# Kernel tuning notes

Hardware: AMD Instinct MI355X
Metric: run time of the kernel (lower is better)

The kernel has to match this reference:

```python
import jax, jax.numpy as jnp
import numpy as np

B, T, D, K = 64, 4096, 90, 32
LOG2PI = 1.8378770664093453


def setup_inputs() -> dict:
    key = jax.random.key(0)
    k1, k2, k3, k4, k5 = jax.random.split(key, 5)
    X = jax.random.normal(k1, (B, T, D), dtype=jnp.float32)
    state_priors = jax.random.uniform(k2, (K,), dtype=jnp.float32)
    transition_matrix = jax.random.uniform(k3, (K, K), dtype=jnp.float32)
    mu = jax.random.normal(k4, (K, D), dtype=jnp.float32) * 0.5
    log_var = jax.random.normal(k5, (K, D), dtype=jnp.float32) * 0.1
    return {"X": X, "state_priors": state_priors,
            "transition_matrix": transition_matrix, "mu": mu, "log_var": log_var}


def _emission_logprobs(X, mu, log_var):
    # Diagonal-Gaussian log density per state: (B,T,K)
    # expand (x-mu)^2*inv_var to avoid materializing a (B,T,K,D) tensor
    inv_var = jnp.exp(-log_var)                                   # (K,D)
    quad = (jnp.einsum('btd,kd->btk', X * X, inv_var)
            - 2.0 * jnp.einsum('btd,kd->btk', X, mu * inv_var)
            + jnp.sum(mu * mu * inv_var, axis=-1))                # (B,T,K)
    return -0.5 * (quad + jnp.sum(log_var, axis=-1) + D * LOG2PI)


def reference(X, state_priors, transition_matrix, mu, log_var):
    log_A = jax.nn.log_softmax(transition_matrix, axis=1)   # (K,K)
    log_pi = jax.nn.log_softmax(state_priors, axis=0)       # (K,)
    em = _emission_logprobs(X, mu, log_var)                 # (B,T,K)

    log_alpha0 = log_pi + em[:, 0, :]                       # (B,K)

    def step(log_alpha, e_t):
        # log_alpha: (B,K), e_t: (B,K)
        la = e_t + jax.nn.logsumexp(log_alpha[:, :, None] + log_A[None], axis=1)
        return la, None

    em_rest = jnp.swapaxes(em[:, 1:, :], 0, 1)              # (T-1,B,K)
    log_alpha_T, _ = jax.lax.scan(step, log_alpha0, em_rest)
    # sum over subjects of logsumexp over states at final timestep
    return jnp.sum(jax.nn.logsumexp(log_alpha_T, axis=-1))
```

## Files before the change

### kernel.cpp

```cpp
#include <hip/hip_runtime.h>
#include <stdint.h>

#define B_ 64
#define T_ 4096
#define D_ 90
#define K_ 32
#define CH_ 32
#define F_  128
#define NB_ 2048

typedef float f32x16 __attribute__((ext_vector_type(16)));
typedef __bf16 bf16x8 __attribute__((ext_vector_type(8)));

#define WS_A     0
#define WS_PI    1024
#define WS_C0    1056
#define WS_WF    1088
#define WS_EACC  4160
#define WS_MS    12352
#define WS_E0    20544
#define WS_Q2    22080

__device__ __forceinline__ int perm_r(int r) {
  int t2 = (r >> 2) & 3;
  return r + ((t2 == 1) ? 4 : (t2 == 2) ? -4 : 0);
}
__device__ __forceinline__ uint32_t pk2(float hi, float lo) {
  return __builtin_amdgcn_perm(__float_as_uint(hi), __float_as_uint(lo), 0x07060302u);
}
__device__ __forceinline__ uint32_t rnd_pk(float hi, float lo) {
  uint32_t uh = __float_as_uint(hi) + 0x8000u;
  uint32_t ul = __float_as_uint(lo) + 0x8000u;
  return __builtin_amdgcn_perm(uh, ul, 0x07060302u);
}
__device__ __forceinline__ float bf2f(ushort u) {
  return __uint_as_float(((uint32_t)u) << 16);
}
__device__ __forceinline__ bf16x8 mkbf(uint32_t a, uint32_t b, uint32_t c, uint32_t d) {
  union { uint32_t u[4]; bf16x8 v; } x;
  x.u[0] = a; x.u[1] = b; x.u[2] = c; x.u[3] = d;
  return x.v;
}

__global__ __launch_bounds__(1024) void prep_kernel(
    const float* __restrict__ priors, const float* __restrict__ trans,
    const float* __restrict__ mu, const float* __restrict__ lv,
    float* __restrict__ ws) {
  int tid = threadIdx.x;
  {
    float v = trans[tid];
    float m = v;
    #pragma unroll
    for (int mk = 16; mk; mk >>= 1) m = fmaxf(m, __shfl_xor(m, mk));
    float e = expf(v - m);
    float s = e;
    #pragma unroll
    for (int mk = 16; mk; mk >>= 1) s += __shfl_xor(s, mk);
    ws[WS_A + tid] = e / s;
  }
  if (tid < 32) {
    float v = priors[tid];
    float m = v;
    #pragma unroll
    for (int mk = 16; mk; mk >>= 1) m = fmaxf(m, __shfl_xor(m, mk));
    float e = expf(v - m);
    float s = e;
    #pragma unroll
    for (int mk = 16; mk; mk >>= 1) s += __shfl_xor(s, mk);
    ws[WS_PI + tid] = e / s;
  }
  for (int i = tid; i < 6144; i += 1024) {
    int j = i & 7, l = (i >> 3) & 63, cm = i >> 9;
    int c = cm >> 1, mat = cm & 1;
    int h = l >> 5, nn = l & 31;
    int d = 16 * c + 8 * h + j;
    float v = 0.0f;
    if (d < D_) {
      float ivd = expf(-lv[nn * D_ + d]);
      v = (mat == 0) ? -0.5f * ivd : mu[nn * D_ + d] * ivd;
    }
    ((ushort*)(ws + WS_WF))[i] = (ushort)((__float_as_uint(v) + 0x8000u) >> 16);
  }
  if (tid < 32) {
    float s = 0.0f;
    for (int d = 0; d < D_; ++d) {
      float l  = lv[tid * D_ + d];
      float iv = expf(-l);
      float m_ = mu[tid * D_ + d];
      s += m_ * m_ * iv + l;
    }
    ws[WS_C0 + tid] = -0.5f * (s + (float)D_ * 1.8378770664093453f);
  }
}

__global__ __launch_bounds__(256, 8) void fused_kernel(const float* __restrict__ X,
                                                       float* __restrict__ ws,
                                                       float* __restrict__ out) {
  __shared__ __align__(16) ushort sh[4][1280];
  __shared__ float msb[4];
  __shared__ int   peb[4];
  int tid = threadIdx.x;
  int l = tid & 63, w = tid >> 6;
  int n = l & 31, h = l >> 5;
  int tB = blockIdx.x << 7;
  int t0 = tB + (w << 5);
  int b  = t0 >> 12;
  if (blockIdx.x == 0 && tid == 0) *out = 0.0f;

  const float* xr = X + (size_t)(t0 + n) * D_;
  const uint4* wfp = (const uint4*)((const ushort*)(ws + WS_WF));
  float c0 = ws[WS_C0 + n];
  f32x16 acc1, acc2;
  #pragma unroll
  for (int r = 0; r < 16; ++r) { acc1[r] = 0.0f; acc2[r] = 0.0f; }
  #pragma unroll
  for (int c = 0; c < 6; ++c) {
    int s = 16 * c + 8 * h;
    union { uint32_t u[4]; bf16x8 v; } xb, x2b;
    #pragma unroll
    for (int p = 0; p < 4; ++p) {
      float2 v2;
      if (s + 2 * p < D_) v2 = *(const float2*)(xr + s + 2 * p);
      else { v2.x = 0.0f; v2.y = 0.0f; }
      xb.u[p]  = rnd_pk(v2.y, v2.x);
      x2b.u[p] = rnd_pk(v2.y * v2.y, v2.x * v2.x);
    }
    union { uint4 u; bf16x8 v; } w1, w2;
    w2.u = wfp[(2 * c) * 64 + l];
    w1.u = wfp[(2 * c + 1) * 64 + l];
    acc1 = __builtin_amdgcn_mfma_f32_32x32x16_bf16(xb.v,  w1.v, acc1, 0, 0, 0);
    acc2 = __builtin_amdgcn_mfma_f32_32x32x16_bf16(x2b.v, w2.v, acc2, 0, 0, 0);
  }
  float em[16], mrow[16];
  #pragma unroll
  for (int r = 0; r < 16; ++r) {
    float v = acc1[r] + acc2[r] + c0;
    em[r] = v;
    float m = v;
    #pragma unroll
    for (int mk = 1; mk <= 16; mk <<= 1) m = fmaxf(m, __shfl_xor(m, mk));
    mrow[r] = m;
  }
  ushort* Ew = sh[w];
  #pragma unroll
  for (int q = 0; q < 4; ++q) {
    float e0 = exp2f((em[4*q]   - mrow[4*q])   * 1.44269504088896f);
    float e1 = exp2f((em[4*q+1] - mrow[4*q+1]) * 1.44269504088896f);
    float e2 = exp2f((em[4*q+2] - mrow[4*q+2]) * 1.44269504088896f);
    float e3 = exp2f((em[4*q+3] - mrow[4*q+3]) * 1.44269504088896f);
    uint2 d;
    d.x = rnd_pk(e1, e0);
    d.y = rnd_pk(e3, e2);
    *(uint2*)(Ew + n * 40 + 8 * q + 4 * h) = d;
    if (q == 0 && h == 0 && (t0 & (T_ - 1)) == 0)
      ((ushort*)(ws + WS_E0))[b * K_ + n] = (ushort)(d.x & 0xFFFF);
  }
  float msum = 0.0f;
  #pragma unroll
  for (int r = 0; r < 16; ++r) msum += mrow[r];
  msum += __shfl_xor(msum, 32);
  if (l == 0) msb[w] = msum;

  int col = perm_r(n);
  const float* A = ws + WS_A;
  float astat[16];
  #pragma unroll
  for (int j = 0; j < 8; ++j) {
    astat[j]     = A[(8 * h + j) * K_ + col];
    astat[8 + j] = A[(16 + 8 * h + j) * K_ + col];
  }
  uint32_t q[8];
  #pragma unroll
  for (int r = 0; r < 4; ++r) {
    int s0 = 8 * h + 2 * r;
    uint32_t lo = (s0 == n)     ? 0x3F80u : 0u;
    uint32_t hi = (s0 + 1 == n) ? 0x3F80u : 0u;
    q[r] = lo | (hi << 16);
    int s2 = s0 + 16;
    lo = (s2 == n)     ? 0x3F80u : 0u;
    hi = (s2 + 1 == n) ? 0x3F80u : 0u;
    q[4 + r] = lo | (hi << 16);
  }
  int eacc = 0;
  const f32x16 z = {0.f,0.f,0.f,0.f,0.f,0.f,0.f,0.f,0.f,0.f,0.f,0.f,0.f,0.f,0.f,0.f};
  f32x16 acc;
  #pragma unroll
  for (int r = 0; r < 16; ++r) acc[r] = 0.0f;

  auto step = [&](float e0) {
    uint32_t au[8];
    #pragma unroll
    for (int r = 0; r < 4; ++r) {
      au[r]     = pk2(astat[2 * r + 1] * e0, astat[2 * r] * e0);
      au[4 + r] = pk2(astat[8 + 2 * r + 1] * e0, astat[8 + 2 * r] * e0);
    }
    bf16x8 alo = mkbf(au[0], au[1], au[2], au[3]);
    bf16x8 ahi = mkbf(au[4], au[5], au[6], au[7]);
    bf16x8 qlo = mkbf(q[0], q[1], q[2], q[3]);
    bf16x8 qhi = mkbf(q[4], q[5], q[6], q[7]);
    acc = __builtin_amdgcn_mfma_f32_32x32x16_bf16(alo, qlo, z, 0, 0, 0);
    acc = __builtin_amdgcn_mfma_f32_32x32x16_bf16(ahi, qhi, acc, 0, 0, 0);
    #pragma unroll
    for (int r = 0; r < 4; ++r) {
      q[r]     = pk2(acc[2 * r + 1], acc[2 * r]);
      q[4 + r] = pk2(acc[8 + 2 * r + 1], acc[8 + 2 * r]);
    }
  };
  auto lmul = [&](uint4 lo, uint4 hi) {
    bf16x8 alo = mkbf(lo.x, lo.y, lo.z, lo.w);
    bf16x8 ahi = mkbf(hi.x, hi.y, hi.z, hi.w);
    bf16x8 qlo = mkbf(q[0], q[1], q[2], q[3]);
    bf16x8 qhi = mkbf(q[4], q[5], q[6], q[7]);
    acc = __builtin_amdgcn_mfma_f32_32x32x16_bf16(alo, qlo, z, 0, 0, 0);
    acc = __builtin_amdgcn_mfma_f32_32x32x16_bf16(ahi, qhi, acc, 0, 0, 0);
    #pragma unroll
    for (int r = 0; r < 4; ++r) {
      q[r]     = pk2(acc[2 * r + 1], acc[2 * r]);
      q[4 + r] = pk2(acc[8 + 2 * r + 1], acc[8 + 2 * r]);
    }
  };
  auto renorm = [&]() {
    float m = acc[0];
    #pragma unroll
    for (int r = 1; r < 16; ++r) m = fmaxf(m, acc[r]);
    #pragma unroll
    for (int mk = 1; mk <= 32; mk <<= 1) m = fmaxf(m, __shfl_xor(m, mk));
    int ex;
    frexpf(m, &ex);
    float sc = ldexpf(1.0f, -ex);
    eacc += ex;
    #pragma unroll
    for (int r = 0; r < 16; ++r) acc[r] *= sc;
    #pragma unroll
    for (int r = 0; r < 4; ++r) {
      q[r]     = pk2(acc[2 * r + 1], acc[2 * r]);
      q[4 + r] = pk2(acc[8 + 2 * r + 1], acc[8 + 2 * r]);
    }
  };

  const ushort* Eb = sh[w] + col * 40;
  int g0 = 0;
  if ((t0 & (T_ - 1)) == 0) {
    uint4 ev = *(const uint4*)(Eb);
    #pragma unroll
    for (int j = 1; j < 8; ++j) {
      uint32_t u = ((const uint32_t*)&ev)[j >> 1];
      step(bf2f((j & 1) ? (ushort)(u >> 16) : (ushort)(u & 0xFFFF)));
    }
    renorm();
    g0 = 1;
  }
  for (int g = g0; g < CH_ / 8; ++g) {
    uint4 ev = *(const uint4*)(Eb + 8 * g);
    #pragma unroll
    for (int j = 0; j < 8; ++j) {
      uint32_t u = ((const uint32_t*)&ev)[j >> 1];
      step(bf2f((j & 1) ? (ushort)(u >> 16) : (ushort)(u & 0xFFFF)));
    }
    renorm();
  }
  ushort* Qw = sh[w];
  #pragma unroll
  for (int r = 0; r < 16; ++r) {
    int m_ = (r & 3) + 8 * (r >> 2) + 4 * h;
    Qw[perm_r(m_) * 40 + n] = (ushort)(__float_as_uint(acc[r]) >> 16);
  }
  if (l == 0) peb[w] = eacc;
  __syncthreads();
  if (w != 0) return;

  #pragma unroll
  for (int r = 0; r < 4; ++r) {
    int s0 = 8 * h + 2 * r;
    uint32_t lo = (s0 == n)     ? 0x3F80u : 0u;
    uint32_t hi = (s0 + 1 == n) ? 0x3F80u : 0u;
    q[r] = lo | (hi << 16);
    int s2 = s0 + 16;
    lo = (s2 == n)     ? 0x3F80u : 0u;
    hi = (s2 + 1 == n) ? 0x3F80u : 0u;
    q[4 + r] = lo | (hi << 16);
  }
  eacc = peb[0] + peb[1] + peb[2] + peb[3];
  float msm = msb[0] + msb[1] + msb[2] + msb[3];
  #pragma unroll
  for (int p = 0; p < 4; ++p) {
    const ushort* base = sh[p] + col * 40;
    uint4 lo = *(const uint4*)(base + 8 * h);
    uint4 hi = *(const uint4*)(base + 16 + 8 * h);
    lmul(lo, hi);
  }
  renorm();
  ushort* Qo = (ushort*)(ws + WS_Q2) + (size_t)blockIdx.x * (K_ * K_);
  #pragma unroll
  for (int r = 0; r < 16; ++r) {
    int m_ = (r & 3) + 8 * (r >> 2) + 4 * h;
    Qo[perm_r(m_) * K_ + n] = (ushort)(__float_as_uint(acc[r]) >> 16);
  }
  if (l == 0) {
    ((int*)ws)[WS_EACC + blockIdx.x] = eacc;
    ws[WS_MS + blockIdx.x] = msm;
  }
}

__global__ __launch_bounds__(256) void combine_kernel(float* __restrict__ ws,
                                                      float* __restrict__ out) {
  __shared__ __align__(16) ushort pm[4][1280];
  __shared__ int pe[4];
  int tid = threadIdx.x;
  int l = tid & 63, w = tid >> 6;
  int h = l >> 5, n = l & 31;
  int b = blockIdx.x;
  int row = perm_r(n);
  int eacc;
  {
    const int* ea = ((const int*)ws) + WS_EACC + b * 32 + w * 8;
    int v = (l < 8) ? ea[l] : 0;
    #pragma unroll
    for (int mk = 1; mk <= 4; mk <<= 1) v += __shfl_xor(v, mk);
    eacc = __shfl(v, 0);
  }
  uint32_t q[8];
  #pragma unroll
  for (int r = 0; r < 4; ++r) {
    int s0 = 8 * h + 2 * r;
    uint32_t lo = (s0 == n)     ? 0x3F80u : 0u;
    uint32_t hi = (s0 + 1 == n) ? 0x3F80u : 0u;
    q[r] = lo | (hi << 16);
    int s2 = s0 + 16;
    lo = (s2 == n)     ? 0x3F80u : 0u;
    hi = (s2 + 1 == n) ? 0x3F80u : 0u;
    q[4 + r] = lo | (hi << 16);
  }
  f32x16 acc;
  #pragma unroll
  for (int r = 0; r < 16; ++r) acc[r] = 0.0f;
  const f32x16 z = {0.f,0.f,0.f,0.f,0.f,0.f,0.f,0.f,0.f,0.f,0.f,0.f,0.f,0.f,0.f,0.f};

  auto lmul = [&](uint4 lo, uint4 hi) {
    bf16x8 alo = mkbf(lo.x, lo.y, lo.z, lo.w);
    bf16x8 ahi = mkbf(hi.x, hi.y, hi.z, hi.w);
    bf16x8 qlo = mkbf(q[0], q[1], q[2], q[3]);
    bf16x8 qhi = mkbf(q[4], q[5], q[6], q[7]);
    acc = __builtin_amdgcn_mfma_f32_32x32x16_bf16(alo, qlo, z, 0, 0, 0);
    acc = __builtin_amdgcn_mfma_f32_32x32x16_bf16(ahi, qhi, acc, 0, 0, 0);
    #pragma unroll
    for (int r = 0; r < 4; ++r) {
      q[r]     = pk2(acc[2 * r + 1], acc[2 * r]);
      q[4 + r] = pk2(acc[8 + 2 * r + 1], acc[8 + 2 * r]);
    }
  };
  auto renorm = [&]() {
    float m = acc[0];
    #pragma unroll
    for (int r = 1; r < 16; ++r) m = fmaxf(m, acc[r]);
    #pragma unroll
    for (int mk = 1; mk <= 32; mk <<= 1) m = fmaxf(m, __shfl_xor(m, mk));
    int ex;
    frexpf(m, &ex);
    float sc = ldexpf(1.0f, -ex);
    eacc += ex;
    #pragma unroll
    for (int r = 0; r < 16; ++r) acc[r] *= sc;
    #pragma unroll
    for (int r = 0; r < 4; ++r) {
      q[r]     = pk2(acc[2 * r + 1], acc[2 * r]);
      q[4 + r] = pk2(acc[8 + 2 * r + 1], acc[8 + 2 * r]);
    }
  };

  const ushort* Qb = (const ushort*)(ws + WS_Q2) + (size_t)(b * 32 + w * 8) * (K_ * K_);
  #pragma unroll
  for (int p = 0; p < 8; ++p) {
    const ushort* Mc = Qb + (size_t)p * (K_ * K_) + row * K_;
    uint4 lo = *(const uint4*)(Mc + 8 * h);
    uint4 hi = *(const uint4*)(Mc + 16 + 8 * h);
    lmul(lo, hi);
    if ((p & 3) == 3) renorm();
  }
  #pragma unroll
  for (int r = 0; r < 16; ++r) {
    int m_ = (r & 3) + 8 * (r >> 2) + 4 * h;
    pm[w][perm_r(m_) * 40 + n] = (ushort)(__float_as_uint(acc[r]) >> 16);
  }
  if (l == 0) pe[w] = eacc;
  __syncthreads();
  if (w != 0) return;

  float alpha0 = ws[WS_PI + n] * bf2f(((const ushort*)(ws + WS_E0))[b * K_ + n]);
  float msm;
  {
    float v = (l < 32) ? ws[WS_MS + b * 32 + l] : 0.0f;
    #pragma unroll
    for (int mk = 1; mk <= 32; mk <<= 1) v += __shfl_xor(v, mk);
    msm = v;
  }
  #pragma unroll
  for (int r = 0; r < 4; ++r) {
    int s0 = 8 * h + 2 * r;
    uint32_t lo = (s0 == n)     ? 0x3F80u : 0u;
    uint32_t hi = (s0 + 1 == n) ? 0x3F80u : 0u;
    q[r] = lo | (hi << 16);
    int s2 = s0 + 16;
    lo = (s2 == n)     ? 0x3F80u : 0u;
    hi = (s2 + 1 == n) ? 0x3F80u : 0u;
    q[4 + r] = lo | (hi << 16);
  }
  #pragma unroll
  for (int r = 0; r < 16; ++r) acc[r] = 0.0f;
  int et = pe[0] + pe[1] + pe[2] + pe[3];
  #pragma unroll
  for (int p = 0; p < 4; ++p) {
    const ushort* base = pm[p] + row * 40;
    uint4 lo = *(const uint4*)(base + 8 * h);
    uint4 hi = *(const uint4*)(base + 16 + 8 * h);
    lmul(lo, hi);
  }
  float part = 0.0f;
  #pragma unroll
  for (int r = 0; r < 16; ++r) part += acc[r];
  part *= alpha0;
  #pragma unroll
  for (int mk = 1; mk <= 32; mk <<= 1) part += __shfl_xor(part, mk);
  if (l == 0) {
    float res = logf(part) + (float)et * 0.69314718055994531f + msm;
    atomicAdd(out, res);
  }
}

extern "C" void kernel_launch(void* const* d_in, const int* in_sizes, int n_in,
                              void* d_out, int out_size, void* d_ws, size_t ws_size,
                              hipStream_t stream) {
  (void)in_sizes; (void)n_in; (void)out_size; (void)ws_size;
  const float* X      = (const float*)d_in[0];
  const float* priors = (const float*)d_in[1];
  const float* trans  = (const float*)d_in[2];
  const float* mu     = (const float*)d_in[3];
  const float* lv     = (const float*)d_in[4];
  float* ws  = (float*)d_ws;
  float* out = (float*)d_out;
  prep_kernel<<<1, 1024, 0, stream>>>(priors, trans, mu, lv, ws);
  fused_kernel<<<NB_, 256, 0, stream>>>(X, ws, out);
  combine_kernel<<<B_, 256, 0, stream>>>(ws, out);
}
```

Measured before the change: 192.6 us.

## Stage X and emission weights through LDS with coalesced loads, shuffle emissions

The emission GEMM now copies the bf16 weight fragments into LDS once per block and stages X through a per-wave LDS buffer using coalesced row-pair loads, double-buffered against the MFMAs. X squared is recomputed from the bf16 values, and the two accumulators are merged into one. The per-step emission values are delivered by cross-lane shuffles from registers instead of an LDS round trip. This aims to fix strided, uncoalesced global reads of X and the repeated weight fetches. In exchange it adds block-wide barriers, more LDS use, and slightly different rounding of x^2, which is now computed from the bf16-rounded x.

```diff
diff --git a/kernel.cpp b/kernel.cpp
--- a/kernel.cpp
+++ b/kernel.cpp
@@ -20,6 +20,10 @@
 #define WS_MS    12352
 #define WS_E0    20544
 #define WS_Q2    22080
+
+#define LDS_XOFF(w) ((w) * 768)
+#define LDS_WF      3072
+#define LDS_TOT     9216
 
 __device__ __forceinline__ int perm_r(int r) {
   int t2 = (r >> 2) & 3;
@@ -96,7 +100,7 @@
 __global__ __launch_bounds__(256, 8) void fused_kernel(const float* __restrict__ X,
                                                        float* __restrict__ ws,
                                                        float* __restrict__ out) {
-  __shared__ __align__(16) ushort sh[4][1280];
+  __shared__ __align__(16) ushort sh[LDS_TOT];
   __shared__ float msb[4];
   __shared__ int   peb[4];
   int tid = threadIdx.x;
@@ -107,59 +111,96 @@
   int b  = t0 >> 12;
   if (blockIdx.x == 0 && tid == 0) *out = 0.0f;
 
-  const float* xr = X + (size_t)(t0 + n) * D_;
-  const uint4* wfp = (const uint4*)((const ushort*)(ws + WS_WF));
+  {
+    const uint4* wfp = (const uint4*)((const ushort*)(ws + WS_WF));
+    uint4* wfl = (uint4*)(sh + LDS_WF);
+    #pragma unroll
+    for (int k = 0; k < 3; ++k) wfl[tid + (k << 8)] = wfp[tid + (k << 8)];
+  }
   float c0 = ws[WS_C0 + n];
-  f32x16 acc1, acc2;
-  #pragma unroll
-  for (int r = 0; r < 16; ++r) { acc1[r] = 0.0f; acc2[r] = 0.0f; }
+
+  int srow = l >> 1, sp = l & 1;
+  const float* xg = X + (size_t)(t0 + srow) * D_ + 8 * sp;
+  ushort* xbuf = sh + LDS_XOFF(w);
+  float2 va[4];
+  auto xload = [&](int c) {
+    #pragma unroll
+    for (int s = 0; s < 4; ++s) {
+      int d = 16 * c + 8 * sp + 2 * s;
+      if (d < D_) va[s] = *(const float2*)(xg + 16 * c + 2 * s);
+      else { va[s].x = 0.0f; va[s].y = 0.0f; }
+    }
+  };
+  auto xwrite = [&]() {
+    uint4 pkv;
+    pkv.x = rnd_pk(va[0].y, va[0].x);
+    pkv.y = rnd_pk(va[1].y, va[1].x);
+    pkv.z = rnd_pk(va[2].y, va[2].x);
+    pkv.w = rnd_pk(va[3].y, va[3].x);
+    *(uint4*)(xbuf + srow * 24 + 8 * sp) = pkv;
+  };
+  xload(0);
+  xwrite();
+  xload(1);
+  __syncthreads();
+
+  const ushort* wfl = sh + LDS_WF;
+  f32x16 acc;
+  #pragma unroll
+  for (int r = 0; r < 16; ++r) acc[r] = 0.0f;
   #pragma unroll
   for (int c = 0; c < 6; ++c) {
-    int s = 16 * c + 8 * h;
-    union { uint32_t u[4]; bf16x8 v; } xb, x2b;
-    #pragma unroll
-    for (int p = 0; p < 4; ++p) {
-      float2 v2;
-      if (s + 2 * p < D_) v2 = *(const float2*)(xr + s + 2 * p);
-      else { v2.x = 0.0f; v2.y = 0.0f; }
-      xb.u[p]  = rnd_pk(v2.y, v2.x);
-      x2b.u[p] = rnd_pk(v2.y * v2.y, v2.x * v2.x);
-    }
+    union { uint4 u; bf16x8 v; } xb;
+    xb.u = *(const uint4*)(xbuf + n * 24 + 8 * h);
+    float x[8];
+    #pragma unroll
+    for (int j = 0; j < 8; ++j) {
+      uint32_t uu = ((const uint32_t*)&xb.u)[j >> 1];
+      x[j] = bf2f((j & 1) ? (ushort)(uu >> 16) : (ushort)(uu & 0xFFFF));
+    }
+    union { uint32_t u[4]; bf16x8 v; } x2b;
+    #pragma unroll
+    for (int r = 0; r < 4; ++r)
+      x2b.u[r] = rnd_pk(x[2*r+1] * x[2*r+1], x[2*r] * x[2*r]);
     union { uint4 u; bf16x8 v; } w1, w2;
-    w2.u = wfp[(2 * c) * 64 + l];
-    w1.u = wfp[(2 * c + 1) * 64 + l];
-    acc1 = __builtin_amdgcn_mfma_f32_32x32x16_bf16(xb.v,  w1.v, acc1, 0, 0, 0);
-    acc2 = __builtin_amdgcn_mfma_f32_32x32x16_bf16(x2b.v, w2.v, acc2, 0, 0, 0);
+    w2.u = *(const uint4*)(wfl + (2 * c)     * 512 + l * 8);
+    w1.u = *(const uint4*)(wfl + (2 * c + 1) * 512 + l * 8);
+    acc = __builtin_amdgcn_mfma_f32_32x32x16_bf16(xb.v,  w1.v, acc, 0, 0, 0);
+    acc = __builtin_amdgcn_mfma_f32_32x32x16_bf16(x2b.v, w2.v, acc, 0, 0, 0);
+    if (c < 5) {
+      xwrite();
+      if (c < 4) xload(c + 2);
+    }
   }
   float em[16], mrow[16];
   #pragma unroll
   for (int r = 0; r < 16; ++r) {
-    float v = acc1[r] + acc2[r] + c0;
+    float v = acc[r] + c0;
     em[r] = v;
     float m = v;
     #pragma unroll
     for (int mk = 1; mk <= 16; mk <<= 1) m = fmaxf(m, __shfl_xor(m, mk));
     mrow[r] = m;
   }
-  ushort* Ew = sh[w];
+  uint32_t ebf[8];
   #pragma unroll
   for (int q = 0; q < 4; ++q) {
     float e0 = exp2f((em[4*q]   - mrow[4*q])   * 1.44269504088896f);
     float e1 = exp2f((em[4*q+1] - mrow[4*q+1]) * 1.44269504088896f);
     float e2 = exp2f((em[4*q+2] - mrow[4*q+2]) * 1.44269504088896f);
     float e3 = exp2f((em[4*q+3] - mrow[4*q+3]) * 1.44269504088896f);
-    uint2 d;
-    d.x = rnd_pk(e1, e0);
-    d.y = rnd_pk(e3, e2);
-    *(uint2*)(Ew + n * 40 + 8 * q + 4 * h) = d;
-    if (q == 0 && h == 0 && (t0 & (T_ - 1)) == 0)
-      ((ushort*)(ws + WS_E0))[b * K_ + n] = (ushort)(d.x & 0xFFFF);
-  }
+    ebf[2*q]     = rnd_pk(e1, e0);
+    ebf[2*q + 1] = rnd_pk(e3, e2);
+  }
+  bool first = ((t0 & (T_ - 1)) == 0);
+  if (first && h == 0)
+    ((ushort*)(ws + WS_E0))[b * K_ + n] = (ushort)(ebf[0] & 0xFFFF);
   float msum = 0.0f;
   #pragma unroll
   for (int r = 0; r < 16; ++r) msum += mrow[r];
   msum += __shfl_xor(msum, 32);
   if (l == 0) msb[w] = msum;
+  __syncthreads();
 
   int col = perm_r(n);
   const float* A = ws + WS_A;
@@ -183,7 +224,6 @@
   }
   int eacc = 0;
   const f32x16 z = {0.f,0.f,0.f,0.f,0.f,0.f,0.f,0.f,0.f,0.f,0.f,0.f,0.f,0.f,0.f,0.f};
-  f32x16 acc;
   #pragma unroll
   for (int r = 0; r < 16; ++r) acc[r] = 0.0f;
 
@@ -238,28 +278,18 @@
     }
   };
 
-  const ushort* Eb = sh[w] + col * 40;
-  int g0 = 0;
-  if ((t0 & (T_ - 1)) == 0) {
-    uint4 ev = *(const uint4*)(Eb);
-    #pragma unroll
-    for (int j = 1; j < 8; ++j) {
-      uint32_t u = ((const uint32_t*)&ev)[j >> 1];
-      step(bf2f((j & 1) ? (ushort)(u >> 16) : (ushort)(u & 0xFFFF)));
-    }
-    renorm();
-    g0 = 1;
-  }
-  for (int g = g0; g < CH_ / 8; ++g) {
-    uint4 ev = *(const uint4*)(Eb + 8 * g);
-    #pragma unroll
-    for (int j = 0; j < 8; ++j) {
-      uint32_t u = ((const uint32_t*)&ev)[j >> 1];
-      step(bf2f((j & 1) ? (ushort)(u >> 16) : (ushort)(u & 0xFFFF)));
-    }
-    renorm();
-  }
-  ushort* Qw = sh[w];
+  int src0 = col, src1 = col + 32;
+  #pragma unroll
+  for (int t = 0; t < 32; ++t) {
+    uint32_t ed = (uint32_t)__shfl((int)ebf[2 * (t >> 3) + ((t >> 1) & 1)],
+                                   ((t >> 2) & 1) ? src1 : src0);
+    float e0 = bf2f((t & 1) ? (ushort)(ed >> 16) : (ushort)(ed & 0xFFFF));
+    if (t > 0) step(e0);
+    else if (!first) step(e0);
+    if ((t & 7) == 7) renorm();
+  }
+
+  ushort* Qw = sh + w * 1280;
   #pragma unroll
   for (int r = 0; r < 16; ++r) {
     int m_ = (r & 3) + 8 * (r >> 2) + 4 * h;
@@ -284,7 +314,7 @@
   float msm = msb[0] + msb[1] + msb[2] + msb[3];
   #pragma unroll
   for (int p = 0; p < 4; ++p) {
-    const ushort* base = sh[p] + col * 40;
+    const ushort* base = sh + p * 1280 + col * 40;
     uint4 lo = *(const uint4*)(base + 8 * h);
     uint4 hi = *(const uint4*)(base + 16 + 8 * h);
     lmul(lo, hi);
```

Result: slower. 197.4 us (+2.5%).
